# Performance work log

Measured on AMD Instinct MI355X. Metric: run time of the kernel, lower is better.

Reference implementation:

```python
import jax, jax.numpy as jnp
import numpy as np

D_MODEL = 2048
N_HEADS = 16
HEAD_DIM = D_MODEL // N_HEADS
ROPE_BASE = 10000.0


def rope(x):
    # x: [b, h, s, d]; matches the torch module exactly:
    # x1 = even dims, x2 = odd dims; output = concat([x1*cos - x2*sin, x1*sin + x2*cos], -1)
    b, h, s, d = x.shape
    theta = 1.0 / ROPE_BASE ** (jnp.arange(0, d, 2, dtype=jnp.float32) / d)  # [d/2]
    angles = jnp.arange(s, dtype=jnp.float32)[:, None] * theta[None, :]       # [s, d/2]
    cos = jnp.cos(angles)[None, None]  # [1,1,s,d/2]
    sin = jnp.sin(angles)[None, None]
    x1, x2 = x[..., ::2], x[..., 1::2]
    return jnp.concatenate([x1 * cos - x2 * sin, x1 * sin + x2 * cos], axis=-1)


def setup_inputs() -> dict:
    key = jax.random.key(0)
    ks = jax.random.split(key, 5)
    b, s = 2, 2048
    x = jax.random.normal(ks[0], (b, s, D_MODEL), dtype=jnp.float32)
    scale_in = 1.0 / np.sqrt(D_MODEL)
    Wqkv = jax.random.normal(ks[1], (D_MODEL, 3 * D_MODEL), dtype=jnp.float32) * scale_in
    bqkv = jnp.zeros((3 * D_MODEL,), dtype=jnp.float32)
    Wo = jax.random.normal(ks[2], (D_MODEL, D_MODEL), dtype=jnp.float32) * scale_in
    bo = jnp.zeros((D_MODEL,), dtype=jnp.float32)
    return {"x": x, "Wqkv": Wqkv, "bqkv": bqkv, "Wo": Wo, "bo": bo}


def reference(x, Wqkv, bqkv, Wo, bo):
    b, s, d = x.shape
    qkv = x @ Wqkv + bqkv                      # [b, s, 3d]
    q, k, v = jnp.split(qkv, 3, axis=-1)
    def to_heads(t):
        return t.reshape(b, s, N_HEADS, HEAD_DIM).transpose(0, 2, 1, 3)  # [b,h,s,hd]
    q, k, v = to_heads(q), to_heads(k), to_heads(v)
    q = rope(q)
    k = rope(k)
    scores = jnp.einsum('bhqd,bhkd->bhqk', q, k) / jnp.sqrt(jnp.float32(HEAD_DIM))
    attn = jax.nn.softmax(scores, axis=-1)
    out = jnp.einsum('bhqk,bhkd->bhqd', attn, v)
    out = out.transpose(0, 2, 1, 3).reshape(b, s, d)
    return out @ Wo + bo
```

## Files before the change

kernel.cpp:

```cpp
#include <hip/hip_runtime.h>
#include <hip/hip_bf16.h>
#include <cstdint>
#include <type_traits>

#define D_MODEL 2048
#define NH 16
#define HD 128
#define SEQ 2048
#define QKV_LD (3 * D_MODEL)

typedef __attribute__((ext_vector_type(8))) short short8;
typedef __attribute__((ext_vector_type(4))) float f32x4;
typedef __attribute__((ext_vector_type(16))) float f32x16;

__device__ __forceinline__ ushort f2bf(float f) {
    union { float f; uint32_t u; } c; c.f = f;
    uint32_t u = c.u;
    uint32_t r = (u + 0x7FFFu + ((u >> 16) & 1u)) >> 16;
    return (ushort)r;
}
__device__ __forceinline__ float bf2f(ushort b) {
    union { uint32_t u; float f; } c; c.u = ((uint32_t)b) << 16;
    return c.f;
}

__global__ void cvt_bf16_kernel(const float* __restrict__ in, ushort* __restrict__ out, int n4) {
    int idx = blockIdx.x * blockDim.x + threadIdx.x;
    if (idx >= n4) return;
    float4 v = ((const float4*)in)[idx];
    ushort4 o;
    o.x = f2bf(v.x); o.y = f2bf(v.y); o.z = f2bf(v.z); o.w = f2bf(v.w);
    ((ushort4*)out)[idx] = o;
}

__global__ void transpose_bf16_kernel(const float* __restrict__ in, ushort* __restrict__ out,
                                      int R, int C) {
    __shared__ float tile[32][33];
    int tx = threadIdx.x, ty = threadIdx.y;
    int c0 = blockIdx.x * 32, r0 = blockIdx.y * 32;
    for (int i = 0; i < 4; ++i) {
        int r = r0 + ty + i * 8;
        tile[ty + i * 8][tx] = in[(size_t)r * C + c0 + tx];
    }
    __syncthreads();
    for (int i = 0; i < 4; ++i) {
        int c = c0 + ty + i * 8;
        out[(size_t)c * R + r0 + tx] = f2bf(tile[tx][ty + i * 8]);
    }
}

template <typename OutT>
__global__ __launch_bounds__(256) void gemm_bt_bias(
    const ushort* __restrict__ A,
    const ushort* __restrict__ Bt,
    const float* __restrict__ bias,
    OutT* __restrict__ C,
    int M, int N, int K)
{
    __shared__ ushort As[128 * 32];
    __shared__ ushort Bs[128 * 32];
    int t = threadIdx.x;
    int m0 = blockIdx.y * 128, n0 = blockIdx.x * 128;
    int wave = t >> 6, lane = t & 63;
    int wm = (wave & 1) * 64, wn = (wave >> 1) * 64;
    int lr = lane & 15, lh = lane >> 4;

    f32x4 acc[4][4];
    for (int i = 0; i < 4; i++)
        for (int j = 0; j < 4; j++)
            acc[i][j] = (f32x4)0.0f;

    int srow = t >> 2;
    int scol = (t & 3) * 8;
    const ushort* Ag = A + (size_t)(m0 + srow) * K + scol;
    const ushort* Bg = Bt + (size_t)(n0 + srow) * K + scol;

    for (int k0 = 0; k0 < K; k0 += 32) {
        __syncthreads();
        {
            uint4 a0 = *(const uint4*)(Ag + k0);
            uint4 a1 = *(const uint4*)(Ag + (size_t)64 * K + k0);
            uint4 b0 = *(const uint4*)(Bg + k0);
            uint4 b1 = *(const uint4*)(Bg + (size_t)64 * K + k0);
            *(uint4*)(As + srow * 32 + scol) = a0;
            *(uint4*)(As + (srow + 64) * 32 + scol) = a1;
            *(uint4*)(Bs + srow * 32 + scol) = b0;
            *(uint4*)(Bs + (srow + 64) * 32 + scol) = b1;
        }
        __syncthreads();
        short8 a[4], b[4];
        for (int i = 0; i < 4; i++)
            a[i] = *(const short8*)(As + (wm + i * 16 + lr) * 32 + lh * 8);
        for (int j = 0; j < 4; j++)
            b[j] = *(const short8*)(Bs + (wn + j * 16 + lr) * 32 + lh * 8);
        for (int i = 0; i < 4; i++)
            for (int j = 0; j < 4; j++)
                acc[i][j] = __builtin_amdgcn_mfma_f32_16x16x32_bf16(a[i], b[j], acc[i][j], 0, 0, 0);
    }

    for (int i = 0; i < 4; i++) {
        int row = m0 + wm + i * 16 + lh * 4;
        for (int j = 0; j < 4; j++) {
            int col = n0 + wn + j * 16 + lr;
            float bv = bias[col];
            for (int r = 0; r < 4; r++) {
                float v = acc[i][j][r] + bv;
                if constexpr (std::is_same<OutT, ushort>::value)
                    C[(size_t)(row + r) * N + col] = f2bf(v);
                else
                    C[(size_t)(row + r) * N + col] = v;
            }
        }
    }
}

__global__ void rope_cast_qk(const ushort* __restrict__ qkv,
                             ushort* __restrict__ Qb, ushort* __restrict__ Kb) {
    int t = threadIdx.x;
    int wv = blockIdx.x * 4 + (t >> 6);
    int j = t & 63;
    int bs = wv >> 5;
    int rem = wv & 31;
    int which = rem >> 4;
    int h = rem & 15;
    int s = bs & 2047;
    int b = bs >> 11;
    size_t src = (size_t)bs * QKV_LD + which * D_MODEL + h * HD;
    uint32_t pr = *(const uint32_t*)(qkv + src + 2 * j);
    float x1 = bf2f((ushort)(pr & 0xffff));
    float x2 = bf2f((ushort)(pr >> 16));
    float theta = powf(10000.0f, -(float)j * (1.0f / 64.0f));
    float ang = (float)s * theta;
    float sn, cs;
    sincosf(ang, &sn, &cs);
    float sc = which ? 1.0f : 0.08838834764831845f;
    float o1 = (x1 * cs - x2 * sn) * sc;
    float o2 = (x1 * sn + x2 * cs) * sc;
    ushort* dst = which ? Kb : Qb;
    size_t obase = ((size_t)(b * NH + h) * SEQ + s) * HD;
    dst[obase + j] = f2bf(o1);
    dst[obase + 64 + j] = f2bf(o2);
}

__global__ void v_transpose(const ushort* __restrict__ qkv, ushort* __restrict__ Vt) {
    __shared__ ushort tile[32][33];
    int tx = threadIdx.x, ty = threadIdx.y;
    int s0 = blockIdx.x * 32;
    int d0 = blockIdx.y * 32;
    int bh = blockIdx.z;
    int b = bh >> 4, h = bh & 15;
    for (int i = 0; i < 4; ++i) {
        int s = s0 + ty + i * 8;
        tile[ty + i * 8][tx] = qkv[((size_t)(b * SEQ + s)) * QKV_LD + 2 * D_MODEL + h * HD + d0 + tx];
    }
    __syncthreads();
    for (int i = 0; i < 4; ++i) {
        int d = d0 + ty + i * 8;
        Vt[((size_t)bh * HD + d) * SEQ + s0 + tx] = tile[tx][ty + i * 8];
    }
}

__global__ __launch_bounds__(256) void attn_mfma(const ushort* __restrict__ Qb,
                                                 const ushort* __restrict__ Kb,
                                                 const ushort* __restrict__ Vt,
                                                 ushort* __restrict__ ctx) {
    __shared__ ushort smem[25600];
    ushort* Ks = smem;
    ushort* Vts = smem + 8192;
    ushort* Ps = smem + 16384;

    int t = threadIdx.x;
    int w = t >> 6, l = t & 63;
    int l31 = l & 31, g = l >> 5;
    int q0 = blockIdx.x * 128;
    int bh = blockIdx.y;
    int b = bh >> 4, h = bh & 15;

    int qrow = q0 + w * 32 + l31;
    const ushort* Qg = Qb + ((size_t)bh * SEQ + qrow) * HD;
    short8 qf[8];
#pragma unroll
    for (int kc = 0; kc < 8; kc++)
        qf[kc] = *(const short8*)(Qg + kc * 16 + g * 8);

    f32x16 O[4];
#pragma unroll
    for (int di = 0; di < 4; di++) O[di] = (f32x16)0.0f;
    float m_run = -INFINITY, l_run = 0.0f;

    const ushort* KgB = Kb + (size_t)bh * SEQ * HD;
    const ushort* VtB = Vt + (size_t)bh * HD * SEQ;

    for (int k0 = 0; k0 < SEQ; k0 += 64) {
        __syncthreads();
#pragma unroll
        for (int c2 = 0; c2 < 4; c2++) {
            int f = c2 * 256 + t;
            int r = f >> 4, c = f & 15;
            int cp = c ^ (r & 15);
            uint4 v = *(const uint4*)(KgB + (size_t)(k0 + r) * HD + c * 8);
            *(uint4*)(Ks + r * 128 + cp * 8) = v;
        }
#pragma unroll
        for (int c2 = 0; c2 < 4; c2++) {
            int f = c2 * 256 + t;
            int d = f >> 3, c = f & 7;
            int cp = c ^ (d & 7);
            uint4 v = *(const uint4*)(VtB + (size_t)d * SEQ + k0 + c * 8);
            *(uint4*)(Vts + d * 64 + cp * 8) = v;
        }
        __syncthreads();

        f32x16 St[2];
        St[0] = (f32x16)0.0f;
        St[1] = (f32x16)0.0f;
#pragma unroll
        for (int ki = 0; ki < 2; ki++) {
            int row = ki * 32 + l31;
#pragma unroll
            for (int kc = 0; kc < 8; kc++) {
                int cp = (kc * 2 + g) ^ (row & 15);
                short8 a = *(const short8*)(Ks + row * 128 + cp * 8);
                St[ki] = __builtin_amdgcn_mfma_f32_32x32x16_bf16(a, qf[kc], St[ki], 0, 0, 0);
            }
        }

        float mx = -INFINITY;
#pragma unroll
        for (int ki = 0; ki < 2; ki++)
#pragma unroll
            for (int r = 0; r < 16; r++) mx = fmaxf(mx, St[ki][r]);
        mx = fmaxf(mx, __shfl_xor(mx, 32));
        float mn = fmaxf(m_run, mx);
        float alpha = __expf(m_run - mn);
        m_run = mn;
        float psum = 0.0f;
#pragma unroll
        for (int ki = 0; ki < 2; ki++)
#pragma unroll
            for (int r = 0; r < 16; r++) {
                float p = __expf(St[ki][r] - mn);
                St[ki][r] = p;
                psum += p;
            }
        psum += __shfl_xor(psum, 32);
        l_run = l_run * alpha + psum;
#pragma unroll
        for (int di = 0; di < 4; di++)
#pragma unroll
            for (int r = 0; r < 16; r++) O[di][r] *= alpha;

        {
            int qloc = w * 32 + l31;
            ushort* Pr = Ps + qloc * 72;
#pragma unroll
            for (int ki = 0; ki < 2; ki++)
#pragma unroll
                for (int u = 0; u < 4; u++) {
                    ushort4 pk;
                    pk.x = f2bf(St[ki][4 * u + 0]);
                    pk.y = f2bf(St[ki][4 * u + 1]);
                    pk.z = f2bf(St[ki][4 * u + 2]);
                    pk.w = f2bf(St[ki][4 * u + 3]);
                    *(ushort4*)(Pr + ki * 32 + 8 * u + 4 * g) = pk;
                }
        }

        {
            int qloc = w * 32 + l31;
            short8 pb[4];
#pragma unroll
            for (int kc = 0; kc < 4; kc++)
                pb[kc] = *(const short8*)(Ps + qloc * 72 + kc * 16 + g * 8);
#pragma unroll
            for (int di = 0; di < 4; di++) {
                int d = di * 32 + l31;
#pragma unroll
                for (int kc = 0; kc < 4; kc++) {
                    int cp = (kc * 2 + g) ^ (d & 7);
                    short8 va = *(const short8*)(Vts + d * 64 + cp * 8);
                    O[di] = __builtin_amdgcn_mfma_f32_32x32x16_bf16(va, pb[kc], O[di], 0, 0, 0);
                }
            }
        }
    }

    __syncthreads();
    float inv = 1.0f / l_run;
    ushort* ob = smem;
    {
        int qloc = w * 32 + l31;
        ushort* orow = ob + qloc * 128;
#pragma unroll
        for (int di = 0; di < 4; di++)
#pragma unroll
            for (int u = 0; u < 4; u++) {
                ushort4 pk;
                pk.x = f2bf(O[di][4 * u + 0] * inv);
                pk.y = f2bf(O[di][4 * u + 1] * inv);
                pk.z = f2bf(O[di][4 * u + 2] * inv);
                pk.w = f2bf(O[di][4 * u + 3] * inv);
                *(ushort4*)(orow + di * 32 + 8 * u + 4 * g) = pk;
            }
    }
#pragma unroll
    for (int p = 0; p < 8; p++) {
        int qloc = w * 32 + p * 4 + (l >> 4);
        int c16 = l & 15;
        uint4 v = *(const uint4*)(ob + qloc * 128 + c16 * 8);
        size_t tok = (size_t)b * SEQ + q0 + qloc;
        *(uint4*)(ctx + tok * D_MODEL + h * HD + c16 * 8) = v;
    }
}

extern "C" void kernel_launch(void* const* d_in, const int* in_sizes, int n_in,
                              void* d_out, int out_size, void* d_ws, size_t ws_size,
                              hipStream_t stream) {
    const float* x    = (const float*)d_in[0];
    const float* Wqkv = (const float*)d_in[1];
    const float* bqkv = (const float*)d_in[2];
    const float* Wo   = (const float*)d_in[3];
    const float* bo   = (const float*)d_in[4];
    float* out = (float*)d_out;

    char* ws = (char*)d_ws;
    ushort* x_bf   = (ushort*)(ws);
    ushort* wqkvT  = (ushort*)(ws + 16777216);
    ushort* woT    = (ushort*)(ws + 41943040);
    ushort* qkv_bf = (ushort*)(ws + 50331648);
    ushort* Qb     = (ushort*)(ws + 100663296);
    ushort* Kb     = (ushort*)(ws + 117440512);
    ushort* VtG    = (ushort*)(ws + 134217728);
    ushort* ctx    = (ushort*)(ws + 150994944);

    cvt_bf16_kernel<<<8192, 256, 0, stream>>>(x, x_bf, 2097152);
    transpose_bf16_kernel<<<dim3(192, 64), dim3(32, 8), 0, stream>>>(Wqkv, wqkvT, 2048, 6144);
    transpose_bf16_kernel<<<dim3(64, 64), dim3(32, 8), 0, stream>>>(Wo, woT, 2048, 2048);
    gemm_bt_bias<ushort><<<dim3(48, 32), 256, 0, stream>>>(x_bf, wqkvT, bqkv, qkv_bf, 4096, 6144, 2048);
    rope_cast_qk<<<32768, 256, 0, stream>>>(qkv_bf, Qb, Kb);
    v_transpose<<<dim3(64, 4, 32), dim3(32, 8), 0, stream>>>(qkv_bf, VtG);
    attn_mfma<<<dim3(16, 32), 256, 0, stream>>>(Qb, Kb, VtG, ctx);
    gemm_bt_bias<float><<<dim3(16, 32), 256, 0, stream>>>(ctx, woT, bo, out, 4096, 2048, 2048);
}
```

Baseline: 476.4 us.

## Load GEMM tiles directly into LDS and precompute the RoPE cos/sin table

The bf16 GEMM now stages A and B tiles with global_load_lds 16-byte direct-to-LDS loads, one contiguous 512-element region per wave. This replaces the global-to-register-to-LDS round trip and frees the VGPRs and ds_write instructions it used. A small new kernel precomputes a per-(position, frequency) cos/sin table into workspace that ctx later reuses, so the RoPE kernel reads it instead of calling powf and sincosf in every thread. The risks are that the direct loads still sit behind a full barrier with no double buffering, and that the table adds an extra launch plus memory reads.

```diff
diff --git a/kernel.cpp b/kernel.cpp
--- a/kernel.cpp
+++ b/kernel.cpp
@@ -22,6 +22,12 @@
 __device__ __forceinline__ float bf2f(ushort b) {
     union { uint32_t u; float f; } c; c.u = ((uint32_t)b) << 16;
     return c.f;
+}
+
+__device__ __forceinline__ void load_lds16(const ushort* g, ushort* l) {
+    __builtin_amdgcn_global_load_lds(
+        (const __attribute__((address_space(1))) void*)g,
+        (__attribute__((address_space(3))) void*)l, 16, 0, 0);
 }
 
 __global__ void cvt_bf16_kernel(const float* __restrict__ in, ushort* __restrict__ out, int n4) {
@@ -57,8 +63,8 @@
     OutT* __restrict__ C,
     int M, int N, int K)
 {
-    __shared__ ushort As[128 * 32];
-    __shared__ ushort Bs[128 * 32];
+    __shared__ __align__(16) ushort As[128 * 32];
+    __shared__ __align__(16) ushort Bs[128 * 32];
     int t = threadIdx.x;
     int m0 = blockIdx.y * 128, n0 = blockIdx.x * 128;
     int wave = t >> 6, lane = t & 63;
@@ -74,19 +80,15 @@
     int scol = (t & 3) * 8;
     const ushort* Ag = A + (size_t)(m0 + srow) * K + scol;
     const ushort* Bg = Bt + (size_t)(n0 + srow) * K + scol;
+    ushort* AsW = As + wave * 512;
+    ushort* BsW = Bs + wave * 512;
 
     for (int k0 = 0; k0 < K; k0 += 32) {
         __syncthreads();
-        {
-            uint4 a0 = *(const uint4*)(Ag + k0);
-            uint4 a1 = *(const uint4*)(Ag + (size_t)64 * K + k0);
-            uint4 b0 = *(const uint4*)(Bg + k0);
-            uint4 b1 = *(const uint4*)(Bg + (size_t)64 * K + k0);
-            *(uint4*)(As + srow * 32 + scol) = a0;
-            *(uint4*)(As + (srow + 64) * 32 + scol) = a1;
-            *(uint4*)(Bs + srow * 32 + scol) = b0;
-            *(uint4*)(Bs + (srow + 64) * 32 + scol) = b1;
-        }
+        load_lds16(Ag + k0, AsW);
+        load_lds16(Ag + (size_t)64 * K + k0, AsW + 2048);
+        load_lds16(Bg + k0, BsW);
+        load_lds16(Bg + (size_t)64 * K + k0, BsW + 2048);
         __syncthreads();
         short8 a[4], b[4];
         for (int i = 0; i < 4; i++)
@@ -114,7 +116,18 @@
     }
 }
 
+__global__ void rope_table(float2* __restrict__ tab) {
+    int i = blockIdx.x * blockDim.x + threadIdx.x;
+    int s = i >> 6, j = i & 63;
+    float theta = powf(10000.0f, -(float)j * (1.0f / 64.0f));
+    float ang = (float)s * theta;
+    float sn, cs;
+    sincosf(ang, &sn, &cs);
+    tab[i] = make_float2(cs, sn);
+}
+
 __global__ void rope_cast_qk(const ushort* __restrict__ qkv,
+                             const float2* __restrict__ tab,
                              ushort* __restrict__ Qb, ushort* __restrict__ Kb) {
     int t = threadIdx.x;
     int wv = blockIdx.x * 4 + (t >> 6);
@@ -129,10 +142,8 @@
     uint32_t pr = *(const uint32_t*)(qkv + src + 2 * j);
     float x1 = bf2f((ushort)(pr & 0xffff));
     float x2 = bf2f((ushort)(pr >> 16));
-    float theta = powf(10000.0f, -(float)j * (1.0f / 64.0f));
-    float ang = (float)s * theta;
-    float sn, cs;
-    sincosf(ang, &sn, &cs);
+    float2 cspair = tab[(s << 6) + j];
+    float cs = cspair.x, sn = cspair.y;
     float sc = which ? 1.0f : 0.08838834764831845f;
     float o1 = (x1 * cs - x2 * sn) * sc;
     float o2 = (x1 * sn + x2 * cs) * sc;
@@ -332,12 +343,14 @@
     ushort* Kb     = (ushort*)(ws + 117440512);
     ushort* VtG    = (ushort*)(ws + 134217728);
     ushort* ctx    = (ushort*)(ws + 150994944);
-
+    float2* rtab   = (float2*)(ws + 150994944);
+
+    rope_table<<<512, 256, 0, stream>>>(rtab);
     cvt_bf16_kernel<<<8192, 256, 0, stream>>>(x, x_bf, 2097152);
     transpose_bf16_kernel<<<dim3(192, 64), dim3(32, 8), 0, stream>>>(Wqkv, wqkvT, 2048, 6144);
     transpose_bf16_kernel<<<dim3(64, 64), dim3(32, 8), 0, stream>>>(Wo, woT, 2048, 2048);
     gemm_bt_bias<ushort><<<dim3(48, 32), 256, 0, stream>>>(x_bf, wqkvT, bqkv, qkv_bf, 4096, 6144, 2048);
-    rope_cast_qk<<<32768, 256, 0, stream>>>(qkv_bf, Qb, Kb);
+    rope_cast_qk<<<32768, 256, 0, stream>>>(qkv_bf, rtab, Qb, Kb);
     v_transpose<<<dim3(64, 4, 32), dim3(32, 8), 0, stream>>>(qkv_bf, VtG);
     attn_mfma<<<dim3(16, 32), 256, 0, stream>>>(Qb, Kb, VtG, ctx);
     gemm_bt_bias<float><<<dim3(16, 32), 256, 0, stream>>>(ctx, woT, bo, out, 4096, 2048, 2048);
```

After: 468.7 us. About the same (-1.6%).
